# Optimization experiments

Measured on AMD Instinct MI355X. Metric: run time of the kernel, lower is better.

## Reference

```python
import jax, jax.numpy as jnp
import numpy as np

B, CIN, COUT, H, W = 16, 128, 128, 64, 64
K1, K2, DIL = 3, 3, 1
PAD0 = DIL * (K1 - 1) // 2
PAD1 = DIL * (K2 - 1) // 2
L = H * W


def setup_inputs() -> dict:
    key = jax.random.key(0)
    k1, k2, k3, k4, k5 = jax.random.split(key, 5)
    x = jax.random.normal(k1, (B, CIN, H, W), dtype=jnp.float32)
    # binary per-pixel mask over kernel taps, broadcast over batch*channels
    mask = (jax.random.uniform(k2, (1, K1 * K2, L)) < 0.5).astype(jnp.float32)
    fan_in = CIN * K1 * K2
    bound = 1.0 / np.sqrt(fan_in)
    weight = jax.random.uniform(k3, (COUT, CIN, K1, K2), jnp.float32, -bound, bound)
    mask_weight = jax.random.uniform(k4, (COUT, K1, K2), jnp.float32, -bound, bound)
    bias = jax.random.uniform(k5, (COUT,), jnp.float32, -bound, bound)
    return {"x": x, "mask": mask, "weight": weight, "mask_weight": mask_weight, "bias": bias}


def reference(x, mask, weight, mask_weight, bias):
    # im2col: [B, CIN*K1*K2, H, W]; channel ordering (cin, k1, k2) matches torch unfold
    patches = jax.lax.conv_general_dilated_patches(
        x, (K1, K2), (1, 1), [(PAD0, PAD0), (PAD1, PAD1)], rhs_dilation=(DIL, DIL))
    p = patches.reshape(B, CIN, K1 * K2, L)
    p = p * mask[:, None, :, :]          # mask [1, K, L] broadcasts over B and CIN
    p = p.reshape(B, CIN * K1 * K2, L)
    out = jnp.einsum('ok,bkl->bol', weight.reshape(COUT, -1), p)
    out = out + bias[None, :, None]
    out = out + jnp.einsum('ok,mkl->mol', mask_weight.reshape(COUT, -1), mask)
    return out.reshape(B, COUT, H, W)
```

## Files before the change

### kernel.cpp

```cpp
#include <hip/hip_runtime.h>
#include <stdint.h>

#define B_    16
#define CIN_  128
#define COUT_ 128
#define H_    64
#define W_    64
#define L_    4096
#define KK_   1152
#define PW_   66
#define PPIX_ (PW_ * PW_)

typedef unsigned short u16;
typedef __bf16 bf16x8 __attribute__((ext_vector_type(8)));
typedef float  floatx4 __attribute__((ext_vector_type(4)));
typedef uint32_t u32x4 __attribute__((ext_vector_type(4)));

typedef const __attribute__((address_space(1))) uint32_t* gptr_t;
typedef __attribute__((address_space(3))) uint32_t*       lptr_t;

__device__ __forceinline__ void async_copy16(const void* g, void* l) {
    __builtin_amdgcn_global_load_lds((gptr_t)g, (lptr_t)l, 16, 0, 0);
}

__device__ __forceinline__ u16 f2bf(float f) {
    uint32_t u = __builtin_bit_cast(uint32_t, f);
    uint32_t r = u + 0x7FFFu + ((u >> 16) & 1u);
    return (u16)(r >> 16);
}

__global__ void lmc_transpose_kernel(const float* __restrict__ x, u16* __restrict__ xTp) {
    __shared__ u16 tile[64][CIN_ + 8];
    const int b   = blockIdx.y;
    const int y   = blockIdx.x;
    const int tid = threadIdx.x;

    {
        const int c  = tid >> 1;
        const int x0 = (tid & 1) * 32;
        const float* src = x + ((size_t)b * CIN_ + c) * L_ + y * 64 + x0;
        #pragma unroll
        for (int j = 0; j < 32; j += 4) {
            float4 v = *reinterpret_cast<const float4*>(src + j);
            tile[x0 + j + 0][c] = f2bf(v.x);
            tile[x0 + j + 1][c] = f2bf(v.y);
            tile[x0 + j + 2][c] = f2bf(v.z);
            tile[x0 + j + 3][c] = f2bf(v.w);
        }
    }
    __syncthreads();

    u16* dstrow = xTp + ((size_t)(b * PW_ + (y + 1)) * PW_) * CIN_;
    {
        const int xx   = tid >> 2;
        const int cseg = (tid & 3) * 32;
        u16* dst = dstrow + (size_t)(xx + 1) * CIN_ + cseg;
        #pragma unroll
        for (int i = 0; i < 32; i += 8) {
            *reinterpret_cast<uint4*>(dst + i) =
                *reinterpret_cast<const uint4*>(&tile[xx][cseg + i]);
        }
    }
    const uint4 z = {0u, 0u, 0u, 0u};
    if (tid < 32) {
        const int pix = (tid >> 4) ? 65 : 0;
        *reinterpret_cast<uint4*>(dstrow + (size_t)pix * CIN_ + (tid & 15) * 8) = z;
    }
    if (y == 0 || y == 63) {
        u16* brow = xTp + ((size_t)(b * PW_ + (y == 0 ? 0 : 65)) * PW_) * CIN_;
        for (int i = tid; i < (PW_ * CIN_) / 8; i += 256)
            reinterpret_cast<uint4*>(brow)[i] = z;
    }
}

__global__ void lmc_prep_kernel(const float* __restrict__ mask, const float* __restrict__ mw,
                                const float* __restrict__ bias, const float* __restrict__ w,
                                float* __restrict__ mb, u16* __restrict__ wb2) {
    const int bid = blockIdx.x, tid = threadIdx.x;
    if (bid < 128) {
        const int o = bid;
        float m[9];
        #pragma unroll
        for (int k = 0; k < 9; ++k) m[k] = mw[o * 9 + k];
        const float bs = bias[o];
        for (int l = tid; l < L_; l += 256) {
            float s = bs;
            #pragma unroll
            for (int k = 0; k < 9; ++k) s += m[k] * mask[k * L_ + l];
            mb[o * L_ + l] = s;
        }
    } else {
        const int base = (bid - 128) * 2304;
        #pragma unroll
        for (int i = 0; i < 9; ++i) {
            const int e = base + i * 256 + tid;
            const int k = e >> 14;
            const int rem = e & 16383;
            const int o = rem >> 7, c = rem & 127;
            wb2[e] = f2bf(w[(size_t)o * KK_ + c * 9 + k]);
        }
    }
}

__global__ __launch_bounds__(512, 2)
void lmc_gemm_kernel(const u16* __restrict__ xTp, const u16* __restrict__ wb2,
                     const float* __restrict__ mask, const float* __restrict__ mb,
                     float* __restrict__ out) {
    __shared__ u16 W_lds[396 * 128];

    const int flat    = blockIdx.x;
    const int logical = (flat & 7) * 32 + (flat >> 3);
    const int b       = logical >> 4;
    const int lt      = logical & 15;
    const int Y       = lt * 4;
    const int l0      = lt * 256;

    const int tid  = threadIdx.x;
    const int lane = tid & 63;
    const int wv   = tid >> 6;
    const int wm   = (wv >> 2) * 64;
    const int wn   = (wv & 3) * 64;
    const int lrow = lane & 15;
    const int quad = lane >> 4;

    {
        const char* xw = (const char*)xTp + ((size_t)(b * PW_ + Y) * PW_) * 256;
        for (int t = wv; t < 99; t += 8) {
            const int p    = t * 4 + quad;
            const int srcc = lrow ^ (p & 7);
            async_copy16(xw + (size_t)p * 256 + srcc * 16,
                         (char*)W_lds + t * 1024);
        }
    }

    int arow[4];
    #pragma unroll
    for (int i = 0; i < 4; ++i)
        arow[i] = (wm + i * 16 + lrow) * 128 + quad * 8;

    bf16x8 af[4][4];
    #pragma unroll
    for (int i = 0; i < 4; ++i)
        #pragma unroll
        for (int ks = 0; ks < 4; ++ks)
            af[i][ks] = *reinterpret_cast<const bf16x8*>(wb2 + arow[i] + ks * 32);

    int pix0[4];
    uint64_t bits = 0;
    #pragma unroll
    for (int j = 0; j < 4; ++j) {
        const int ll = wn + j * 16 + lrow;
        pix0[j] = ((ll >> 6) + 1) * 66 + (ll & 63) + 1;
        const int lg = l0 + ll;
        #pragma unroll
        for (int k = 0; k < 9; ++k)
            if (mask[k * L_ + lg] != 0.0f) bits |= (1ull << (k * 4 + j));
    }

    floatx4 acc[4][4];
    #pragma unroll
    for (int i = 0; i < 4; ++i)
        #pragma unroll
        for (int j = 0; j < 4; ++j)
            acc[i][j] = (floatx4){0.f, 0.f, 0.f, 0.f};

    __syncthreads();

    for (int k = 0; k < 9; ++k) {
        const int dy = k / 3 - 1;
        const int dx = k - (k / 3) * 3 - 1;
        const int sh = dy * 66 + dx;
        const int kn = (k < 8) ? k + 1 : 8;
        const u16* wkn = wb2 + kn * 16384;

        uint32_t kp[4];
        #pragma unroll
        for (int j = 0; j < 4; ++j)
            kp[j] = 0u - (uint32_t)((bits >> (k * 4 + j)) & 1ull);

        #pragma unroll
        for (int ks = 0; ks < 4; ++ks) {
            bf16x8 bfr[4];
            #pragma unroll
            for (int j = 0; j < 4; ++j) {
                const int pix  = pix0[j] + sh;
                const int slot = (ks * 4 + quad) ^ (pix & 7);
                bf16x8 v = *reinterpret_cast<const bf16x8*>(&W_lds[pix * 128 + slot * 8]);
                u32x4 t = __builtin_bit_cast(u32x4, v);
                t &= kp[j];
                bfr[j] = __builtin_bit_cast(bf16x8, t);
            }
            #pragma unroll
            for (int i = 0; i < 4; ++i)
                #pragma unroll
                for (int j = 0; j < 4; ++j)
                    acc[i][j] = __builtin_amdgcn_mfma_f32_16x16x32_bf16(af[i][ks], bfr[j], acc[i][j], 0, 0, 0);
            #pragma unroll
            for (int i = 0; i < 4; ++i)
                af[i][ks] = *reinterpret_cast<const bf16x8*>(wkn + arow[i] + ks * 32);
        }
    }

    #pragma unroll
    for (int i = 0; i < 4; ++i) {
        #pragma unroll
        for (int j = 0; j < 4; ++j) {
            const int l = l0 + wn + j * 16 + lrow;
            #pragma unroll
            for (int r = 0; r < 4; ++r) {
                const int o = wm + i * 16 + quad * 4 + r;
                out[((size_t)b * COUT_ + o) * L_ + l] = acc[i][j][r] + mb[o * L_ + l];
            }
        }
    }
}

extern "C" void kernel_launch(void* const* d_in, const int* in_sizes, int n_in,
                              void* d_out, int out_size, void* d_ws, size_t ws_size,
                              hipStream_t stream) {
    const float* x      = (const float*)d_in[0];
    const float* mask   = (const float*)d_in[1];
    const float* weight = (const float*)d_in[2];
    const float* mw     = (const float*)d_in[3];
    const float* bias   = (const float*)d_in[4];
    float* out = (float*)d_out;

    char* ws = (char*)d_ws;
    u16*   xTp = (u16*)ws;
    u16*   wb2 = (u16*)(ws + 17842176);
    float* mb  = (float*)(ws + 17842176 + 294912);

    lmc_transpose_kernel<<<dim3(64, B_), 256, 0, stream>>>(x, xTp);
    lmc_prep_kernel<<<192, 256, 0, stream>>>(mask, mw, bias, weight, mb, wb2);
    lmc_gemm_kernel<<<dim3(256), 512, 0, stream>>>(xTp, wb2, mask, mb, out);
}
```

Measured before the change: 143.3 us.

## Stage weight tiles through double-buffered LDS and merge prep kernels into one launch

The GEMM kernel no longer loads weight fragments directly from global memory into registers. It now copies half-K weight tiles asynchronously into a double-buffered LDS region, prefetching the next tile while the current one is consumed, with a block barrier after each of the 18 steps. The transpose kernel is also merged into the prep kernel, which removes one launch. The cost is extra LDS use and more barriers, which could lower occupancy at two blocks per CU and add sync stalls.

```diff
diff --git a/kernel.cpp b/kernel.cpp
--- a/kernel.cpp
+++ b/kernel.cpp
@@ -29,56 +29,55 @@
     return (u16)(r >> 16);
 }
 
-__global__ void lmc_transpose_kernel(const float* __restrict__ x, u16* __restrict__ xTp) {
-    __shared__ u16 tile[64][CIN_ + 8];
-    const int b   = blockIdx.y;
-    const int y   = blockIdx.x;
-    const int tid = threadIdx.x;
-
-    {
-        const int c  = tid >> 1;
-        const int x0 = (tid & 1) * 32;
-        const float* src = x + ((size_t)b * CIN_ + c) * L_ + y * 64 + x0;
-        #pragma unroll
-        for (int j = 0; j < 32; j += 4) {
-            float4 v = *reinterpret_cast<const float4*>(src + j);
-            tile[x0 + j + 0][c] = f2bf(v.x);
-            tile[x0 + j + 1][c] = f2bf(v.y);
-            tile[x0 + j + 2][c] = f2bf(v.z);
-            tile[x0 + j + 3][c] = f2bf(v.w);
-        }
-    }
-    __syncthreads();
-
-    u16* dstrow = xTp + ((size_t)(b * PW_ + (y + 1)) * PW_) * CIN_;
-    {
-        const int xx   = tid >> 2;
-        const int cseg = (tid & 3) * 32;
-        u16* dst = dstrow + (size_t)(xx + 1) * CIN_ + cseg;
-        #pragma unroll
-        for (int i = 0; i < 32; i += 8) {
-            *reinterpret_cast<uint4*>(dst + i) =
-                *reinterpret_cast<const uint4*>(&tile[xx][cseg + i]);
-        }
-    }
-    const uint4 z = {0u, 0u, 0u, 0u};
-    if (tid < 32) {
-        const int pix = (tid >> 4) ? 65 : 0;
-        *reinterpret_cast<uint4*>(dstrow + (size_t)pix * CIN_ + (tid & 15) * 8) = z;
-    }
-    if (y == 0 || y == 63) {
-        u16* brow = xTp + ((size_t)(b * PW_ + (y == 0 ? 0 : 65)) * PW_) * CIN_;
-        for (int i = tid; i < (PW_ * CIN_) / 8; i += 256)
-            reinterpret_cast<uint4*>(brow)[i] = z;
-    }
-}
-
-__global__ void lmc_prep_kernel(const float* __restrict__ mask, const float* __restrict__ mw,
+__global__ void lmc_prep_kernel(const float* __restrict__ x,
+                                const float* __restrict__ mask, const float* __restrict__ mw,
                                 const float* __restrict__ bias, const float* __restrict__ w,
-                                float* __restrict__ mb, u16* __restrict__ wb2) {
+                                u16* __restrict__ xTp, float* __restrict__ mb,
+                                u16* __restrict__ wb2) {
     const int bid = blockIdx.x, tid = threadIdx.x;
-    if (bid < 128) {
-        const int o = bid;
+    if (bid < 1024) {
+        __shared__ u16 tile[64][CIN_ + 8];
+        const int b = bid >> 6;
+        const int y = bid & 63;
+
+        {
+            const int c  = tid >> 1;
+            const int x0 = (tid & 1) * 32;
+            const float* src = x + ((size_t)b * CIN_ + c) * L_ + y * 64 + x0;
+            #pragma unroll
+            for (int j = 0; j < 32; j += 4) {
+                float4 v = *reinterpret_cast<const float4*>(src + j);
+                tile[x0 + j + 0][c] = f2bf(v.x);
+                tile[x0 + j + 1][c] = f2bf(v.y);
+                tile[x0 + j + 2][c] = f2bf(v.z);
+                tile[x0 + j + 3][c] = f2bf(v.w);
+            }
+        }
+        __syncthreads();
+
+        u16* dstrow = xTp + ((size_t)(b * PW_ + (y + 1)) * PW_) * CIN_;
+        {
+            const int xx   = tid >> 2;
+            const int cseg = (tid & 3) * 32;
+            u16* dst = dstrow + (size_t)(xx + 1) * CIN_ + cseg;
+            #pragma unroll
+            for (int i = 0; i < 32; i += 8) {
+                *reinterpret_cast<uint4*>(dst + i) =
+                    *reinterpret_cast<const uint4*>(&tile[xx][cseg + i]);
+            }
+        }
+        const uint4 z = {0u, 0u, 0u, 0u};
+        if (tid < 32) {
+            const int pix = (tid >> 4) ? 65 : 0;
+            *reinterpret_cast<uint4*>(dstrow + (size_t)pix * CIN_ + (tid & 15) * 8) = z;
+        }
+        if (y == 0 || y == 63) {
+            u16* brow = xTp + ((size_t)(b * PW_ + (y == 0 ? 0 : 65)) * PW_) * CIN_;
+            for (int i = tid; i < (PW_ * CIN_) / 8; i += 256)
+                reinterpret_cast<uint4*>(brow)[i] = z;
+        }
+    } else if (bid < 1152) {
+        const int o = bid - 1024;
         float m[9];
         #pragma unroll
         for (int k = 0; k < 9; ++k) m[k] = mw[o * 9 + k];
@@ -90,7 +89,7 @@
             mb[o * L_ + l] = s;
         }
     } else {
-        const int base = (bid - 128) * 2304;
+        const int base = (bid - 1152) * 2304;
         #pragma unroll
         for (int i = 0; i < 9; ++i) {
             const int e = base + i * 256 + tid;
@@ -107,6 +106,7 @@
                      const float* __restrict__ mask, const float* __restrict__ mb,
                      float* __restrict__ out) {
     __shared__ u16 W_lds[396 * 128];
+    __shared__ u16 A_lds[2][128 * 64];
 
     const int flat    = blockIdx.x;
     const int logical = (flat & 7) * 32 + (flat >> 3);
@@ -123,6 +123,9 @@
     const int lrow = lane & 15;
     const int quad = lane >> 4;
 
+    const char* wb2_c = (const char*)wb2;
+    char* A_c = (char*)A_lds;
+
     {
         const char* xw = (const char*)xTp + ((size_t)(b * PW_ + Y) * PW_) * 256;
         for (int t = wv; t < 99; t += 8) {
@@ -133,17 +136,11 @@
         }
     }
 
-    int arow[4];
-    #pragma unroll
-    for (int i = 0; i < 4; ++i)
-        arow[i] = (wm + i * 16 + lrow) * 128 + quad * 8;
-
-    bf16x8 af[4][4];
-    #pragma unroll
-    for (int i = 0; i < 4; ++i)
-        #pragma unroll
-        for (int ks = 0; ks < 4; ++ks)
-            af[i][ks] = *reinterpret_cast<const bf16x8*>(wb2 + arow[i] + ks * 32);
+    const int ao  = (lane >> 3);
+    const int ach = (lane & 7) ^ (ao & 7);
+    const int aoff0 = (8 * wv + ao) * 256 + ach * 16;
+    async_copy16(wb2_c + aoff0,         A_c + wv * 1024);
+    async_copy16(wb2_c + aoff0 + 16384, A_c + wv * 1024 + 8192);
 
     int pix0[4];
     uint64_t bits = 0;
@@ -166,39 +163,52 @@
 
     __syncthreads();
 
-    for (int k = 0; k < 9; ++k) {
-        const int dy = k / 3 - 1;
-        const int dx = k - (k / 3) * 3 - 1;
-        const int sh = dy * 66 + dx;
-        const int kn = (k < 8) ? k + 1 : 8;
-        const u16* wkn = wb2 + kn * 16384;
-
+    for (int g = 0; g < 18; ++g) {
+        const int k = g >> 1;
+
+        if (g < 17) {
+            const int gn   = g + 1;
+            const int koff = (gn >> 1) * 32768 + (gn & 1) * 128;
+            char* dstb = A_c + (gn & 1) * 16384;
+            async_copy16(wb2_c + koff + aoff0,         dstb + wv * 1024);
+            async_copy16(wb2_c + koff + aoff0 + 16384, dstb + wv * 1024 + 8192);
+        }
+
+        const int sh = (k / 3 - 1) * 66 + (k % 3) - 1;
         uint32_t kp[4];
         #pragma unroll
         for (int j = 0; j < 4; ++j)
             kp[j] = 0u - (uint32_t)((bits >> (k * 4 + j)) & 1ull);
 
-        #pragma unroll
-        for (int ks = 0; ks < 4; ++ks) {
-            bf16x8 bfr[4];
+        const u16* Ac = (const u16*)(A_c + (g & 1) * 16384);
+
+        #pragma unroll
+        for (int ksl = 0; ksl < 2; ++ksl) {
+            const int ksg = (g & 1) * 2 + ksl;
+            bf16x8 af[4], bf[4];
+            #pragma unroll
+            for (int i = 0; i < 4; ++i) {
+                const int orow = wm + i * 16 + lrow;
+                const int slot = (ksl * 4 + quad) ^ (orow & 7);
+                af[i] = *reinterpret_cast<const bf16x8*>(&Ac[orow * 64 + slot * 8]);
+            }
             #pragma unroll
             for (int j = 0; j < 4; ++j) {
                 const int pix  = pix0[j] + sh;
-                const int slot = (ks * 4 + quad) ^ (pix & 7);
+                const int slot = (ksg * 4 + quad) ^ (pix & 7);
                 bf16x8 v = *reinterpret_cast<const bf16x8*>(&W_lds[pix * 128 + slot * 8]);
                 u32x4 t = __builtin_bit_cast(u32x4, v);
                 t &= kp[j];
-                bfr[j] = __builtin_bit_cast(bf16x8, t);
+                bf[j] = __builtin_bit_cast(bf16x8, t);
             }
             #pragma unroll
             for (int i = 0; i < 4; ++i)
                 #pragma unroll
                 for (int j = 0; j < 4; ++j)
-                    acc[i][j] = __builtin_amdgcn_mfma_f32_16x16x32_bf16(af[i][ks], bfr[j], acc[i][j], 0, 0, 0);
-            #pragma unroll
-            for (int i = 0; i < 4; ++i)
-                af[i][ks] = *reinterpret_cast<const bf16x8*>(wkn + arow[i] + ks * 32);
-        }
+                    acc[i][j] = __builtin_amdgcn_mfma_f32_16x16x32_bf16(
+                        af[i], bf[j], acc[i][j], 0, 0, 0);
+        }
+        __syncthreads();
     }
 
     #pragma unroll
@@ -230,7 +240,6 @@
     u16*   wb2 = (u16*)(ws + 17842176);
     float* mb  = (float*)(ws + 17842176 + 294912);
 
-    lmc_transpose_kernel<<<dim3(64, B_), 256, 0, stream>>>(x, xTp);
-    lmc_prep_kernel<<<192, 256, 0, stream>>>(mask, mw, bias, weight, mb, wb2);
-    lmc_gemm_kernel<<<dim3(256), 512, 0, stream>>>(xTp, wb2, mask, mb, out);
-}
+    lmc_prep_kernel<<<1216, 256, 0, stream>>>(x, mask, mw, bias, weight, xTp, mb, wb2);
+    lmc_gemm_kernel<<<256, 512, 0, stream>>>(xTp, wb2, mask, mb, out);
+}
```

Result: faster. 123.5 us (-13.9%).
